# Kernel tuning notes

Hardware: AMD Instinct MI355X
Metric: run time of the kernel (lower is better)

The kernel has to match this reference:

```python
import jax, jax.numpy as jnp
import numpy as np

N = 8192
DIM_IN = 1024
DIM_INNER = 1024
DIM_OUT = 1024


def setup_inputs() -> dict:
    key = jax.random.key(0)
    k1, k2, k3, k4 = jax.random.split(key, 4)
    x = jax.random.normal(k1, (N, DIM_IN), dtype=jnp.float32)
    # torch nn.Linear weights, stored transposed for right-multiplication
    Wqkv = jax.random.normal(k2, (DIM_IN, 3 * DIM_INNER), dtype=jnp.float32) * (DIM_IN ** -0.5)
    Wout = jax.random.normal(k3, (DIM_INNER, DIM_OUT), dtype=jnp.float32) * (DIM_INNER ** -0.5)
    bout = jax.random.normal(k4, (DIM_OUT,), dtype=jnp.float32) * 0.01
    return {"x": x, "Wqkv": Wqkv, "Wout": Wout, "bout": bout}


def reference(x, Wqkv, Wout, bout):
    scale = DIM_INNER ** -0.5
    qkv = x @ Wqkv                      # [N, 3*Di]
    q, k, v = jnp.split(qkv, 3, axis=-1)  # each [N, Di]
    sim = jnp.einsum('id,jd->ij', q, k) * scale  # [N, N]
    # causal mask: future positions (j > i) filled with -finfo.max
    i = jnp.arange(sim.shape[0])[:, None]
    j = jnp.arange(sim.shape[1])[None, :]
    sim = jnp.where(j > i, -jnp.finfo(sim.dtype).max, sim)
    attn = jax.nn.softmax(sim, axis=-1)
    out = jnp.einsum('ij,jd->id', attn, v)  # [N, Di]
    return out @ Wout + bout            # [N, Do]
```

## Files before the change

### kernel.cpp

```cpp
#include <hip/hip_runtime.h>
#include <hip/hip_bf16.h>


typedef __bf16 v8bf __attribute__((ext_vector_type(8)));
typedef float  v4f  __attribute__((ext_vector_type(4)));

struct __align__(8) S4 { short x, y, z, w; };

__device__ inline short f2bf(float f) {
  __hip_bfloat16 h = __float2bfloat16(f);
  return *reinterpret_cast<short*>(&h);
}
__device__ inline float bf2f(short s) {
  unsigned u = ((unsigned)(unsigned short)s) << 16;
  float f;
  __builtin_memcpy(&f, &u, 4);
  return f;
}

__device__ inline void stage_tile(const short* gbase, int ldg, short* lds, int tid) {
#pragma unroll
  for (int p = 0; p < 2; ++p) {
    const int c = p * 256 + tid;
    const int pos = (c & 3) ^ ((c >> 3) & 3);
    const short* g = gbase + (size_t)(c >> 2) * ldg + pos * 8;
    short* l = lds + p * 2048 + (tid >> 6) * 512;
    __builtin_amdgcn_global_load_lds(
        (__attribute__((address_space(1))) void*)(void*)g,
        (__attribute__((address_space(3))) void*)l, 16, 0, 0);
  }
}

__device__ inline void mma_step(const short* As, const short* Bs, v4f acc[4][4],
                                int lane, int wm, int wn) {
  const int qd = lane >> 4, r16 = lane & 15;
  const int sw = (qd ^ ((r16 >> 1) & 3)) * 8;
  const short* ab = As + (wm * 64 + r16) * 32 + sw;
  const short* bb = Bs + (wn * 64 + r16) * 32 + sw;
  v8bf a[4], b[4];
#pragma unroll
  for (int t = 0; t < 4; ++t) {
    a[t] = *(const v8bf*)(ab + t * 512);
    b[t] = *(const v8bf*)(bb + t * 512);
  }
#pragma unroll
  for (int mt = 0; mt < 4; ++mt)
#pragma unroll
    for (int nt = 0; nt < 4; ++nt)
      acc[mt][nt] = __builtin_amdgcn_mfma_f32_16x16x32_bf16(a[mt], b[nt], acc[mt][nt], 0, 0, 0);
}

#define ACC_INIT(acc)                              \
  _Pragma("unroll") for (int i_ = 0; i_ < 4; ++i_) \
  _Pragma("unroll") for (int j_ = 0; j_ < 4; ++j_) \
      acc[i_][j_] = (v4f){0.f, 0.f, 0.f, 0.f};

__global__ __launch_bounds__(256) void k_zerof(float* __restrict__ p, int n) {
  const int i = blockIdx.x * 256 + threadIdx.x;
  if (i < n) p[i] = 0.f;
}

__global__ __launch_bounds__(256) void k_detect(const unsigned short* __restrict__ xs,
                                                int* __restrict__ flag) {
  __shared__ int cnt;
  if (threadIdx.x == 0) cnt = 0;
  __syncthreads();
  int local = 0;
  for (int i = threadIdx.x; i < 4096; i += 256) {
    const unsigned e = (xs[i] >> 7) & 0xFFu;
    if (e >= 0xC0u) ++local;
  }
  if (local) atomicAdd(&cnt, local);
  __syncthreads();
  if (threadIdx.x == 0) *flag = (cnt > 8) ? 1 : 0;
}

__global__ __launch_bounds__(256) void k_convert(const void* __restrict__ in,
                                                 short* __restrict__ out, int n,
                                                 const int* __restrict__ flag) {
  const int stride = gridDim.x * blockDim.x;
  int i = blockIdx.x * blockDim.x + threadIdx.x;
  if (*flag != 0) {
    const float* p = (const float*)in;
    for (; i < n; i += stride) out[i] = f2bf(p[i]);
  } else {
    const short* p = (const short*)in;
    for (; i < n; i += stride) out[i] = p[i];
  }
}

__global__ __launch_bounds__(256) void k_to_f32(const void* __restrict__ in,
                                                float* __restrict__ out, int n,
                                                const int* __restrict__ flag) {
  const int stride = gridDim.x * blockDim.x;
  int i = blockIdx.x * blockDim.x + threadIdx.x;
  if (*flag != 0) {
    const float* p = (const float*)in;
    for (; i < n; i += stride) out[i] = p[i];
  } else {
    const short* p = (const short*)in;
    for (; i < n; i += stride) out[i] = bf2f(p[i]);
  }
}

__global__ __launch_bounds__(256) void k_convT(const void* __restrict__ in,
                                               short* __restrict__ out, int R, int C,
                                               const int* __restrict__ flag) {
  __shared__ short t[32][33];
  const int xx = threadIdx.x & 31, y0 = threadIdx.x >> 5;
  const int c0 = blockIdx.x * 32, r0 = blockIdx.y * 32;
  if (*flag != 0) {
    const float* p = (const float*)in;
#pragma unroll
    for (int i = 0; i < 4; ++i) {
      int r = y0 + i * 8;
      t[r][xx] = f2bf(p[(size_t)(r0 + r) * C + c0 + xx]);
    }
  } else {
    const short* p = (const short*)in;
#pragma unroll
    for (int i = 0; i < 4; ++i) {
      int r = y0 + i * 8;
      t[r][xx] = p[(size_t)(r0 + r) * C + c0 + xx];
    }
  }
  __syncthreads();
#pragma unroll
  for (int i = 0; i < 4; ++i) {
    int r = y0 + i * 8;
    out[(size_t)(c0 + r) * R + r0 + xx] = t[xx][r];
  }
}

__global__ __launch_bounds__(256) void k_gemm_qkv(const short* __restrict__ x,
                                                  const short* __restrict__ wt,
                                                  short* __restrict__ qk,
                                                  short* __restrict__ vT) {
  __shared__ short As[4096], Bs[4096];
  const int tid = threadIdx.x, lane = tid & 63, wave = tid >> 6;
  const int wm = wave >> 1, wn = wave & 1;
  const int m0 = blockIdx.x * 128, n0 = blockIdx.y * 128;
  v4f acc[4][4];
  ACC_INIT(acc)
  for (int k0 = 0; k0 < 1024; k0 += 32) {
    __syncthreads();
    stage_tile(x + (size_t)m0 * 1024 + k0, 1024, As, tid);
    stage_tile(wt + (size_t)n0 * 1024 + k0, 1024, Bs, tid);
    __syncthreads();
    mma_step(As, Bs, acc, lane, wm, wn);
  }
  const int qd = lane >> 4, c16 = lane & 15;
#pragma unroll
  for (int mt = 0; mt < 4; ++mt) {
    const int rl = wm * 64 + mt * 16 + qd * 4;
#pragma unroll
    for (int nt = 0; nt < 4; ++nt) {
      const int cl = wn * 64 + nt * 16 + c16;
      const int n = n0 + cl;
      if (n < 2048) {
#pragma unroll
        for (int r = 0; r < 4; ++r)
          qk[(size_t)(m0 + rl + r) * 2048 + n] = f2bf(acc[mt][nt][r]);
      } else {
        S4 p;
        p.x = f2bf(acc[mt][nt][0]);
        p.y = f2bf(acc[mt][nt][1]);
        p.z = f2bf(acc[mt][nt][2]);
        p.w = f2bf(acc[mt][nt][3]);
        *reinterpret_cast<S4*>(vT + (size_t)(n - 2048) * 8192 + (m0 + rl)) = p;
      }
    }
  }
}

__global__ __launch_bounds__(256) void k_qk_exp(const short* __restrict__ qk,
                                                short* __restrict__ E,
                                                float* __restrict__ l) {
  __shared__ short As[4096], Bs[4096];
  __shared__ float srow[128][2];
  const int tid = threadIdx.x, lane = tid & 63, wave = tid >> 6;
  const int wm = wave >> 1, wn = wave & 1;
  const int b = (int)blockIdx.x;
  int I = (int)((sqrtf(8.f * (float)b + 1.f) - 1.f) * 0.5f);
  while ((I + 1) * (I + 2) / 2 <= b) ++I;
  while (I * (I + 1) / 2 > b) --I;
  const int J = b - I * (I + 1) / 2;
  const int m0 = I * 128, n0 = J * 128;
  v4f acc[4][4];
  ACC_INIT(acc)
  for (int k0 = 0; k0 < 1024; k0 += 32) {
    __syncthreads();
    stage_tile(qk + (size_t)m0 * 2048 + k0, 2048, As, tid);
    stage_tile(qk + 1024 + (size_t)n0 * 2048 + k0, 2048, Bs, tid);
    __syncthreads();
    mma_step(As, Bs, acc, lane, wm, wn);
  }
  short* tb = E + (size_t)(I * (I + 1) / 2 + J) * 16384;
  const int qd = lane >> 4, c16 = lane & 15;
  float rp[4][4];
#pragma unroll
  for (int mt = 0; mt < 4; ++mt)
#pragma unroll
    for (int r = 0; r < 4; ++r) rp[mt][r] = 0.f;
#pragma unroll
  for (int mt = 0; mt < 4; ++mt) {
    const int rl = wm * 64 + mt * 16 + qd * 4;
#pragma unroll
    for (int nt = 0; nt < 4; ++nt) {
      const int cl = wn * 64 + nt * 16 + c16;
      const int gj = n0 + cl;
      const int jj = cl >> 5, qdc = (cl >> 3) & 3, jl = cl & 7;
      short* dst = tb + (((wm * 4 + jj) * 4 + mt) * 512) + qdc * 128 + jl;
#pragma unroll
      for (int r = 0; r < 4; ++r) {
        const int gi = m0 + rl + r;
        const float s = fminf(acc[mt][nt][r] * 0.03125f, 60.f);
        const float e = (gj > gi) ? 0.f : __expf(s);
        dst[(qd * 4 + r) * 8] = f2bf(e);
        rp[mt][r] += e;
      }
    }
  }
#pragma unroll
  for (int mt = 0; mt < 4; ++mt)
#pragma unroll
    for (int r = 0; r < 4; ++r) {
      float v = rp[mt][r];
      v += __shfl_xor(v, 1);
      v += __shfl_xor(v, 2);
      v += __shfl_xor(v, 4);
      v += __shfl_xor(v, 8);
      rp[mt][r] = v;
    }
  if ((lane & 15) == 0) {
#pragma unroll
    for (int mt = 0; mt < 4; ++mt)
#pragma unroll
      for (int r = 0; r < 4; ++r)
        srow[wm * 64 + mt * 16 + qd * 4 + r][wn] = rp[mt][r];
  }
  __syncthreads();
  if (tid < 128) atomicAdd(&l[m0 + tid], srow[tid][0] + srow[tid][1]);
}

__device__ __forceinline__ void pv_loadA(v8bf a[2][4], const short* __restrict__ Et,
                                         int wave, int lane) {
#pragma unroll
  for (int f = 0; f < 2; ++f) {
    const int fi = wave * 2 + f;
    const int wm_ = fi >> 2, mt_ = fi & 3;
#pragma unroll
    for (int jj = 0; jj < 4; ++jj) {
      const int BLK = (wm_ * 4 + jj) * 4 + mt_;
      a[f][jj] = *(const v8bf*)(Et + BLK * 512 + lane * 8);
    }
  }
}

__device__ __forceinline__ void pv_stageV(const short* __restrict__ vbJ,
                                          short* __restrict__ lds, int tid) {
#pragma unroll
  for (int p = 0; p < 8; ++p) {
    const int c = p * 256 + tid;
    const int row = c >> 4;
    const int kc = (c & 15) ^ (row & 15);
    const short* g = vbJ + (size_t)row * 8192 + kc * 8;
    short* lp = lds + (p * 256 + (tid >> 6) * 64) * 8;
    __builtin_amdgcn_global_load_lds(
        (__attribute__((address_space(1))) void*)(void*)g,
        (__attribute__((address_space(3))) void*)lp, 16, 0, 0);
  }
}

__device__ __forceinline__ void pv_compute(const v8bf a[2][4], const short* __restrict__ Vbuf,
                                           v4f acc[2][8], int qd, int r16) {
#pragma unroll
  for (int jj = 0; jj < 4; ++jj) {
    v8bf b[8];
#pragma unroll
    for (int u = 0; u < 8; ++u) {
      const int row = u * 16 + r16;
      const int kc = (jj * 4 + qd) ^ r16;
      b[u] = *(const v8bf*)(Vbuf + row * 128 + kc * 8);
    }
#pragma unroll
    for (int f = 0; f < 2; ++f)
#pragma unroll
      for (int u = 0; u < 8; ++u)
        acc[f][u] = __builtin_amdgcn_mfma_f32_16x16x32_bf16(a[f][jj], b[u], acc[f][u], 0, 0, 0);
  }
}

__global__ __launch_bounds__(256) void k_pv(const short* __restrict__ E,
                                            const short* __restrict__ vT,
                                            const float* __restrict__ l,
                                            short* __restrict__ attn) {
  __shared__ short Vb[2][16384];
  const int tid = threadIdx.x, lane = tid & 63, wave = tid >> 6;
  const int bx = (int)blockIdx.x;
  const int n0 = (int)blockIdx.y * 128;
  const int qd = lane >> 4, r16 = lane & 15;
  const short* vb = vT + (size_t)n0 * 8192;
  for (int half = 0; half < 2; ++half) {
    const int I = half ? 63 - bx : bx;
    const int m0 = I * 128;
    const short* Erow = E + (size_t)(I * (I + 1) / 2) * 16384;
    v4f acc[2][8];
#pragma unroll
    for (int f = 0; f < 2; ++f)
#pragma unroll
      for (int u = 0; u < 8; ++u) acc[f][u] = (v4f){0.f, 0.f, 0.f, 0.f};
    v8bf aA[2][4], aB[2][4];
    __syncthreads();
    pv_stageV(vb, Vb[0], tid);
    pv_loadA(aA, Erow, wave, lane);
    __syncthreads();
    for (int J = 0;; J += 2) {
      if (J + 1 <= I) {
        pv_loadA(aB, Erow + (size_t)(J + 1) * 16384, wave, lane);
        pv_stageV(vb + (J + 1) * 128, Vb[1], tid);
      }
      pv_compute(aA, Vb[0], acc, qd, r16);
      if (J + 1 > I) break;
      __syncthreads();
      if (J + 2 <= I) {
        pv_loadA(aA, Erow + (size_t)(J + 2) * 16384, wave, lane);
        pv_stageV(vb + (J + 2) * 128, Vb[0], tid);
      }
      pv_compute(aB, Vb[1], acc, qd, r16);
      if (J + 2 > I) break;
      __syncthreads();
    }
    const int c16 = lane & 15;
#pragma unroll
    for (int f = 0; f < 2; ++f) {
      const int rbase = wave * 32 + f * 16 + qd * 4;
      float inv[4];
#pragma unroll
      for (int r = 0; r < 4; ++r) inv[r] = 1.0f / fmaxf(l[m0 + rbase + r], 1e-30f);
#pragma unroll
      for (int u = 0; u < 8; ++u) {
#pragma unroll
        for (int r = 0; r < 4; ++r)
          attn[(size_t)(m0 + rbase + r) * 1024 + n0 + u * 16 + c16] = f2bf(acc[f][u][r] * inv[r]);
      }
    }
  }
}

__global__ __launch_bounds__(256) void k_gemm_out(const short* __restrict__ attn,
                                                  const short* __restrict__ wt,
                                                  const float* __restrict__ bout,
                                                  float* __restrict__ out) {
  __shared__ short As[4096], Bs[4096];
  const int tid = threadIdx.x, lane = tid & 63, wave = tid >> 6;
  const int wm = wave >> 1, wn = wave & 1;
  const int m0 = blockIdx.x * 128, n0 = blockIdx.y * 128;
  v4f acc[4][4];
  ACC_INIT(acc)
  for (int k0 = 0; k0 < 1024; k0 += 32) {
    __syncthreads();
    stage_tile(attn + (size_t)m0 * 1024 + k0, 1024, As, tid);
    stage_tile(wt + (size_t)n0 * 1024 + k0, 1024, Bs, tid);
    __syncthreads();
    mma_step(As, Bs, acc, lane, wm, wn);
  }
  const int qd = lane >> 4, c16 = lane & 15;
#pragma unroll
  for (int mt = 0; mt < 4; ++mt) {
    const int rl = wm * 64 + mt * 16 + qd * 4;
#pragma unroll
    for (int nt = 0; nt < 4; ++nt) {
      const int cl = wn * 64 + nt * 16 + c16;
      const float bias = bout[n0 + cl];
#pragma unroll
      for (int r = 0; r < 4; ++r)
        out[(size_t)(m0 + rl + r) * 1024 + n0 + cl] = acc[mt][nt][r] + bias;
    }
  }
}

extern "C" void kernel_launch(void* const* d_in, const int* in_sizes, int n_in,
                              void* d_out, int out_size, void* d_ws, size_t ws_size,
                              hipStream_t stream) {
  (void)out_size; (void)ws_size;
  const void *x = d_in[0], *Wqkv = d_in[1], *Wout = d_in[2], *bout = d_in[3];
  for (int i = 0; i < n_in; ++i) {
    switch (in_sizes[i]) {
      case 8192 * 1024: x = d_in[i]; break;
      case 1024 * 3072: Wqkv = d_in[i]; break;
      case 1024 * 1024: Wout = d_in[i]; break;
      case 1024:        bout = d_in[i]; break;
      default: break;
    }
  }

  char* ws = (char*)d_ws;
  short* qk    = (short*)(ws);
  short* vT    = (short*)(ws + 33554432);
  short* E     = (short*)(ws + 50331648);
  short* xb    = (short*)(ws + 118489088);
  short* attn  = xb;
  short* WqT   = (short*)(ws + 135266304);
  short* WoT   = (short*)(ws + 141557760);
  float* boutf = (float*)(ws + 143654912);
  float* lsum  = (float*)(ws + 143659008);
  int*   flag  = (int*)  (ws + 143691776);

  k_detect<<<1, 256, 0, stream>>>((const unsigned short*)x, flag);
  k_zerof<<<32, 256, 0, stream>>>(lsum, 8192);
  k_convert<<<1024, 256, 0, stream>>>(x, xb, 8192 * 1024, flag);
  k_to_f32<<<1, 256, 0, stream>>>(bout, boutf, 1024, flag);
  k_convT<<<dim3(96, 32), 256, 0, stream>>>(Wqkv, WqT, 1024, 3072, flag);
  k_convT<<<dim3(32, 32), 256, 0, stream>>>(Wout, WoT, 1024, 1024, flag);
  k_gemm_qkv<<<dim3(64, 24), 256, 0, stream>>>(xb, WqT, qk, vT);
  k_qk_exp<<<dim3(2080), 256, 0, stream>>>(qk, E, lsum);
  k_pv<<<dim3(32, 8), 256, 0, stream>>>(E, vT, lsum, attn);
  k_gemm_out<<<dim3(64, 8), 256, 0, stream>>>(attn, WoT, boutf, (float*)d_out);
}
```

Before: 402.9 us.

## Double GEMM K-tile depth to 64 and widen PV kernel to 512 threads

The three tiled GEMM kernels now stage 64-wide K slices per iteration instead of 32, using a new 8-way XOR swizzle. This halves the number of barrier pairs per block at the cost of doubling LDS per block. The PV kernel moves to 512 threads, with each wave handling one 16-row fragment instead of two. That cuts accumulator registers per thread and adds more waves for latency hiding, though the same V tile is now read from LDS by twice as many waves.

```diff
diff --git a/kernel.cpp b/kernel.cpp
--- a/kernel.cpp
+++ b/kernel.cpp
@@ -18,36 +18,40 @@
   return f;
 }
 
-__device__ inline void stage_tile(const short* gbase, int ldg, short* lds, int tid) {
-#pragma unroll
-  for (int p = 0; p < 2; ++p) {
+__device__ inline void stage_tile64(const short* gbase, int ldg, short* lds, int tid) {
+#pragma unroll
+  for (int p = 0; p < 4; ++p) {
     const int c = p * 256 + tid;
-    const int pos = (c & 3) ^ ((c >> 3) & 3);
-    const short* g = gbase + (size_t)(c >> 2) * ldg + pos * 8;
-    short* l = lds + p * 2048 + (tid >> 6) * 512;
+    const int row = c >> 3;
+    const int pos = (c & 7) ^ (row & 7);
+    const short* g = gbase + (size_t)row * ldg + pos * 8;
+    short* l = lds + (p * 256 + (tid >> 6) * 64) * 8;
     __builtin_amdgcn_global_load_lds(
         (__attribute__((address_space(1))) void*)(void*)g,
         (__attribute__((address_space(3))) void*)l, 16, 0, 0);
   }
 }
 
-__device__ inline void mma_step(const short* As, const short* Bs, v4f acc[4][4],
-                                int lane, int wm, int wn) {
+__device__ inline void mma_step64(const short* As, const short* Bs, v4f acc[4][4],
+                                  int lane, int wm, int wn) {
   const int qd = lane >> 4, r16 = lane & 15;
-  const int sw = (qd ^ ((r16 >> 1) & 3)) * 8;
-  const short* ab = As + (wm * 64 + r16) * 32 + sw;
-  const short* bb = Bs + (wn * 64 + r16) * 32 + sw;
-  v8bf a[4], b[4];
-#pragma unroll
-  for (int t = 0; t < 4; ++t) {
-    a[t] = *(const v8bf*)(ab + t * 512);
-    b[t] = *(const v8bf*)(bb + t * 512);
-  }
-#pragma unroll
-  for (int mt = 0; mt < 4; ++mt)
-#pragma unroll
-    for (int nt = 0; nt < 4; ++nt)
-      acc[mt][nt] = __builtin_amdgcn_mfma_f32_16x16x32_bf16(a[mt], b[nt], acc[mt][nt], 0, 0, 0);
+#pragma unroll
+  for (int kh = 0; kh < 2; ++kh) {
+    const int sw = (((kh << 2) | qd) ^ (r16 & 7)) * 8;
+    const short* ab = As + (wm * 64 + r16) * 64 + sw;
+    const short* bb = Bs + (wn * 64 + r16) * 64 + sw;
+    v8bf a[4], b[4];
+#pragma unroll
+    for (int t = 0; t < 4; ++t) {
+      a[t] = *(const v8bf*)(ab + t * 1024);
+      b[t] = *(const v8bf*)(bb + t * 1024);
+    }
+#pragma unroll
+    for (int mt = 0; mt < 4; ++mt)
+#pragma unroll
+      for (int nt = 0; nt < 4; ++nt)
+        acc[mt][nt] = __builtin_amdgcn_mfma_f32_16x16x32_bf16(a[mt], b[nt], acc[mt][nt], 0, 0, 0);
+  }
 }
 
 #define ACC_INIT(acc)                              \
@@ -136,18 +140,18 @@
                                                   const short* __restrict__ wt,
                                                   short* __restrict__ qk,
                                                   short* __restrict__ vT) {
-  __shared__ short As[4096], Bs[4096];
+  __shared__ short As[8192], Bs[8192];
   const int tid = threadIdx.x, lane = tid & 63, wave = tid >> 6;
   const int wm = wave >> 1, wn = wave & 1;
   const int m0 = blockIdx.x * 128, n0 = blockIdx.y * 128;
   v4f acc[4][4];
   ACC_INIT(acc)
-  for (int k0 = 0; k0 < 1024; k0 += 32) {
-    __syncthreads();
-    stage_tile(x + (size_t)m0 * 1024 + k0, 1024, As, tid);
-    stage_tile(wt + (size_t)n0 * 1024 + k0, 1024, Bs, tid);
-    __syncthreads();
-    mma_step(As, Bs, acc, lane, wm, wn);
+  for (int k0 = 0; k0 < 1024; k0 += 64) {
+    __syncthreads();
+    stage_tile64(x + (size_t)m0 * 1024 + k0, 1024, As, tid);
+    stage_tile64(wt + (size_t)n0 * 1024 + k0, 1024, Bs, tid);
+    __syncthreads();
+    mma_step64(As, Bs, acc, lane, wm, wn);
   }
   const int qd = lane >> 4, c16 = lane & 15;
 #pragma unroll
@@ -176,7 +180,7 @@
 __global__ __launch_bounds__(256) void k_qk_exp(const short* __restrict__ qk,
                                                 short* __restrict__ E,
                                                 float* __restrict__ l) {
-  __shared__ short As[4096], Bs[4096];
+  __shared__ short As[8192], Bs[8192];
   __shared__ float srow[128][2];
   const int tid = threadIdx.x, lane = tid & 63, wave = tid >> 6;
   const int wm = wave >> 1, wn = wave & 1;
@@ -188,12 +192,12 @@
   const int m0 = I * 128, n0 = J * 128;
   v4f acc[4][4];
   ACC_INIT(acc)
-  for (int k0 = 0; k0 < 1024; k0 += 32) {
-    __syncthreads();
-    stage_tile(qk + (size_t)m0 * 2048 + k0, 2048, As, tid);
-    stage_tile(qk + 1024 + (size_t)n0 * 2048 + k0, 2048, Bs, tid);
-    __syncthreads();
-    mma_step(As, Bs, acc, lane, wm, wn);
+  for (int k0 = 0; k0 < 1024; k0 += 64) {
+    __syncthreads();
+    stage_tile64(qk + (size_t)m0 * 2048 + k0, 2048, As, tid);
+    stage_tile64(qk + 1024 + (size_t)n0 * 2048 + k0, 2048, Bs, tid);
+    __syncthreads();
+    mma_step64(As, Bs, acc, lane, wm, wn);
   }
   short* tb = E + (size_t)(I * (I + 1) / 2 + J) * 16384;
   const int qd = lane >> 4, c16 = lane & 15;
@@ -243,37 +247,33 @@
   if (tid < 128) atomicAdd(&l[m0 + tid], srow[tid][0] + srow[tid][1]);
 }
 
-__device__ __forceinline__ void pv_loadA(v8bf a[2][4], const short* __restrict__ Et,
-                                         int wave, int lane) {
-#pragma unroll
-  for (int f = 0; f < 2; ++f) {
-    const int fi = wave * 2 + f;
-    const int wm_ = fi >> 2, mt_ = fi & 3;
-#pragma unroll
-    for (int jj = 0; jj < 4; ++jj) {
-      const int BLK = (wm_ * 4 + jj) * 4 + mt_;
-      a[f][jj] = *(const v8bf*)(Et + BLK * 512 + lane * 8);
-    }
-  }
-}
-
-__device__ __forceinline__ void pv_stageV(const short* __restrict__ vbJ,
-                                          short* __restrict__ lds, int tid) {
-#pragma unroll
-  for (int p = 0; p < 8; ++p) {
-    const int c = p * 256 + tid;
+__device__ __forceinline__ void pv_loadA8(v8bf a[4], const short* __restrict__ Et,
+                                          int wave, int lane) {
+  const int wm_ = wave >> 2, mt_ = wave & 3;
+#pragma unroll
+  for (int jj = 0; jj < 4; ++jj) {
+    const int BLK = (wm_ * 4 + jj) * 4 + mt_;
+    a[jj] = *(const v8bf*)(Et + BLK * 512 + lane * 8);
+  }
+}
+
+__device__ __forceinline__ void pv_stageV8(const short* __restrict__ vbJ,
+                                           short* __restrict__ lds, int tid) {
+#pragma unroll
+  for (int p = 0; p < 4; ++p) {
+    const int c = p * 512 + tid;
     const int row = c >> 4;
     const int kc = (c & 15) ^ (row & 15);
     const short* g = vbJ + (size_t)row * 8192 + kc * 8;
-    short* lp = lds + (p * 256 + (tid >> 6) * 64) * 8;
+    short* lp = lds + (p * 512 + (tid >> 6) * 64) * 8;
     __builtin_amdgcn_global_load_lds(
         (__attribute__((address_space(1))) void*)(void*)g,
         (__attribute__((address_space(3))) void*)lp, 16, 0, 0);
   }
 }
 
-__device__ __forceinline__ void pv_compute(const v8bf a[2][4], const short* __restrict__ Vbuf,
-                                           v4f acc[2][8], int qd, int r16) {
+__device__ __forceinline__ void pv_compute8(const v8bf a[4], const short* __restrict__ Vbuf,
+                                            v4f acc[8], int qd, int r16) {
 #pragma unroll
   for (int jj = 0; jj < 4; ++jj) {
     v8bf b[8];
@@ -284,14 +284,12 @@
       b[u] = *(const v8bf*)(Vbuf + row * 128 + kc * 8);
     }
 #pragma unroll
-    for (int f = 0; f < 2; ++f)
-#pragma unroll
-      for (int u = 0; u < 8; ++u)
-        acc[f][u] = __builtin_amdgcn_mfma_f32_16x16x32_bf16(a[f][jj], b[u], acc[f][u], 0, 0, 0);
-  }
-}
-
-__global__ __launch_bounds__(256) void k_pv(const short* __restrict__ E,
+    for (int u = 0; u < 8; ++u)
+      acc[u] = __builtin_amdgcn_mfma_f32_16x16x32_bf16(a[jj], b[u], acc[u], 0, 0, 0);
+  }
+}
+
+__global__ __launch_bounds__(512) void k_pv(const short* __restrict__ E,
                                             const short* __restrict__ vT,
                                             const float* __restrict__ l,
                                             short* __restrict__ attn) {
@@ -305,45 +303,39 @@
     const int I = half ? 63 - bx : bx;
     const int m0 = I * 128;
     const short* Erow = E + (size_t)(I * (I + 1) / 2) * 16384;
-    v4f acc[2][8];
-#pragma unroll
-    for (int f = 0; f < 2; ++f)
-#pragma unroll
-      for (int u = 0; u < 8; ++u) acc[f][u] = (v4f){0.f, 0.f, 0.f, 0.f};
-    v8bf aA[2][4], aB[2][4];
-    __syncthreads();
-    pv_stageV(vb, Vb[0], tid);
-    pv_loadA(aA, Erow, wave, lane);
+    v4f acc[8];
+#pragma unroll
+    for (int u = 0; u < 8; ++u) acc[u] = (v4f){0.f, 0.f, 0.f, 0.f};
+    v8bf aA[4], aB[4];
+    __syncthreads();
+    pv_stageV8(vb, Vb[0], tid);
+    pv_loadA8(aA, Erow, wave, lane);
     __syncthreads();
     for (int J = 0;; J += 2) {
       if (J + 1 <= I) {
-        pv_loadA(aB, Erow + (size_t)(J + 1) * 16384, wave, lane);
-        pv_stageV(vb + (J + 1) * 128, Vb[1], tid);
+        pv_loadA8(aB, Erow + (size_t)(J + 1) * 16384, wave, lane);
+        pv_stageV8(vb + (J + 1) * 128, Vb[1], tid);
       }
-      pv_compute(aA, Vb[0], acc, qd, r16);
+      pv_compute8(aA, Vb[0], acc, qd, r16);
       if (J + 1 > I) break;
       __syncthreads();
       if (J + 2 <= I) {
-        pv_loadA(aA, Erow + (size_t)(J + 2) * 16384, wave, lane);
-        pv_stageV(vb + (J + 2) * 128, Vb[0], tid);
+        pv_loadA8(aA, Erow + (size_t)(J + 2) * 16384, wave, lane);
+        pv_stageV8(vb + (J + 2) * 128, Vb[0], tid);
       }
-      pv_compute(aB, Vb[1], acc, qd, r16);
+      pv_compute8(aB, Vb[1], acc, qd, r16);
       if (J + 2 > I) break;
       __syncthreads();
     }
-    const int c16 = lane & 15;
-#pragma unroll
-    for (int f = 0; f < 2; ++f) {
-      const int rbase = wave * 32 + f * 16 + qd * 4;
-      float inv[4];
-#pragma unroll
-      for (int r = 0; r < 4; ++r) inv[r] = 1.0f / fmaxf(l[m0 + rbase + r], 1e-30f);
-#pragma unroll
-      for (int u = 0; u < 8; ++u) {
-#pragma unroll
-        for (int r = 0; r < 4; ++r)
-          attn[(size_t)(m0 + rbase + r) * 1024 + n0 + u * 16 + c16] = f2bf(acc[f][u][r] * inv[r]);
-      }
+    const int rbase = wave * 16 + qd * 4;
+    float inv[4];
+#pragma unroll
+    for (int r = 0; r < 4; ++r) inv[r] = 1.0f / fmaxf(l[m0 + rbase + r], 1e-30f);
+#pragma unroll
+    for (int u = 0; u < 8; ++u) {
+#pragma unroll
+      for (int r = 0; r < 4; ++r)
+        attn[(size_t)(m0 + rbase + r) * 1024 + n0 + u * 16 + r16] = f2bf(acc[u][r] * inv[r]);
     }
   }
 }
@@ -352,18 +344,18 @@
                                                   const short* __restrict__ wt,
                                                   const float* __restrict__ bout,
                                                   float* __restrict__ out) {
-  __shared__ short As[4096], Bs[4096];
+  __shared__ short As[8192], Bs[8192];
   const int tid = threadIdx.x, lane = tid & 63, wave = tid >> 6;
   const int wm = wave >> 1, wn = wave & 1;
   const int m0 = blockIdx.x * 128, n0 = blockIdx.y * 128;
   v4f acc[4][4];
   ACC_INIT(acc)
-  for (int k0 = 0; k0 < 1024; k0 += 32) {
-    __syncthreads();
-    stage_tile(attn + (size_t)m0 * 1024 + k0, 1024, As, tid);
-    stage_tile(wt + (size_t)n0 * 1024 + k0, 1024, Bs, tid);
-    __syncthreads();
-    mma_step(As, Bs, acc, lane, wm, wn);
+  for (int k0 = 0; k0 < 1024; k0 += 64) {
+    __syncthreads();
+    stage_tile64(attn + (size_t)m0 * 1024 + k0, 1024, As, tid);
+    stage_tile64(wt + (size_t)n0 * 1024 + k0, 1024, Bs, tid);
+    __syncthreads();
+    mma_step64(As, Bs, acc, lane, wm, wn);
   }
   const int qd = lane >> 4, c16 = lane & 15;
 #pragma unroll
@@ -415,6 +407,6 @@
   k_convT<<<dim3(32, 32), 256, 0, stream>>>(Wout, WoT, 1024, 1024, flag);
   k_gemm_qkv<<<dim3(64, 24), 256, 0, stream>>>(xb, WqT, qk, vT);
   k_qk_exp<<<dim3(2080), 256, 0, stream>>>(qk, E, lsum);
-  k_pv<<<dim3(32, 8), 256, 0, stream>>>(E, vT, lsum, attn);
+  k_pv<<<dim3(32, 8), 512, 0, stream>>>(E, vT, lsum, attn);
   k_gemm_out<<<dim3(64, 8), 256, 0, stream>>>(attn, WoT, boutf, (float*)d_out);
 }
```

Measured after the change: 416.4 us. +3.4%, slower.
